# Optimization experiments

Measured on AMD Instinct MI355X. Metric: run time of the kernel, lower is better.

Reference implementation:

```python
import jax, jax.numpy as jnp
import numpy as np

N = 100000
E = 1600000
IN_F, HID, OUT = 64, 128, 64


def setup_inputs() -> dict:
    key = jax.random.key(0)
    ks = jax.random.split(key, 16)
    glorot = lambda k, shp: jax.random.normal(k, shp, jnp.float32) * (2.0 / (shp[0] + shp[1])) ** 0.5
    return {
        "features": jax.random.normal(ks[0], (N, IN_F), jnp.float32),
        "W_neigh1": glorot(ks[1], (IN_F, HID)),
        "W_self1": glorot(ks[2], (IN_F, HID)),
        "b1": jnp.zeros((HID,), jnp.float32),
        "W_neigh2": glorot(ks[3], (HID, HID)),
        "W_self2": glorot(ks[4], (HID, HID)),
        "b2": jnp.zeros((HID,), jnp.float32),
        "Wm1": glorot(ks[5], (HID, HID)),
        "bm1": jnp.zeros((HID,), jnp.float32),
        "Wm2": glorot(ks[6], (HID, OUT)),
        "bm2": jnp.zeros((OUT,), jnp.float32),
        "src": jax.random.randint(ks[7], (E,), 0, N, jnp.int64),
        "dst": jax.random.randint(ks[8], (E,), 0, N, jnp.int64),
    }


def _sage_conv(x, src, dst, W_neigh, W_self, b):
    # mean aggregation of in-neighbor messages (DGL SAGEConv 'mean')
    msg = x[src]                                            # [E, d]
    agg = jax.ops.segment_sum(msg, dst, num_segments=N)     # [N, d]
    deg = jax.ops.segment_sum(jnp.ones((E,), x.dtype), dst, num_segments=N)
    h_neigh = agg / jnp.maximum(deg, 1.0)[:, None]
    return x @ W_self + h_neigh @ W_neigh + b


def reference(features, W_neigh1, W_self1, b1, W_neigh2, W_self2, b2,
              Wm1, bm1, Wm2, bm2, src, dst):
    x = jax.nn.relu(_sage_conv(features, src, dst, W_neigh1, W_self1, b1))
    x = jax.nn.relu(_sage_conv(x, src, dst, W_neigh2, W_self2, b2))
    x = jax.nn.relu(x @ Wm1 + bm1)
    return x @ Wm2 + bm2
```

## Files before the change

kernel.cpp:

```cpp
#include <hip/hip_runtime.h>
#include <hip/hip_fp8.h>

#define N_IN 64
#define HID 128
#define OUT_F 64
#define EPB 6144
#define BKT 128

typedef unsigned short ushort_t;
typedef unsigned char  uchar_t;
typedef unsigned long long ull_t;
typedef ushort_t us8  __attribute__((ext_vector_type(8)));
typedef uchar_t  uc8  __attribute__((ext_vector_type(8)));
typedef short    s16x8 __attribute__((ext_vector_type(8)));
typedef float    f32x4 __attribute__((ext_vector_type(4)));
typedef unsigned int uint2v __attribute__((ext_vector_type(2)));

__device__ inline ushort_t f2bf(float f) {
    unsigned u = __float_as_uint(f);
    u = u + 0x7fffu + ((u >> 16) & 1u);
    return (ushort_t)(u >> 16);
}
__device__ inline float bf2f(ushort_t b) {
    return __uint_as_float((unsigned)b << 16);
}
__device__ inline uchar_t f2fp8(float v) {
    __hip_fp8_e4m3 q(v);
    return (uchar_t)q.__x;
}
__device__ inline void fp8x4_to_f32(unsigned int dw, float* o) {
#if __has_builtin(__builtin_amdgcn_cvt_pk_f32_fp8)
    auto lo = __builtin_amdgcn_cvt_pk_f32_fp8(dw, false);
    auto hi = __builtin_amdgcn_cvt_pk_f32_fp8(dw, true);
    o[0] = lo[0]; o[1] = lo[1]; o[2] = hi[0]; o[3] = hi[1];
#else
#pragma unroll
    for (int i = 0; i < 4; ++i) {
        __hip_fp8_e4m3 h; h.__x = (dw >> (8 * i)) & 0xff;
        o[i] = (float)h;
    }
#endif
}

__global__ __launch_bounds__(256)
void prep_kernel(const float* __restrict__ feat, ushort_t* __restrict__ featb,
                 uchar_t* __restrict__ featq, int n8,
                 const float* __restrict__ Ws1, const float* __restrict__ Wn1,
                 const float* __restrict__ Ws2, const float* __restrict__ Wn2,
                 const float* __restrict__ Wm1, const float* __restrict__ Wm2,
                 ushort_t* __restrict__ wsT1, ushort_t* __restrict__ wnT1,
                 ushort_t* __restrict__ wsT2, ushort_t* __restrict__ wnT2,
                 ushort_t* __restrict__ wmT1, ushort_t* __restrict__ wmT2,
                 const int* __restrict__ dst, int* __restrict__ histT,
                 int E, int nbuk, int nba, int BA, int BB) {
    __shared__ int hist[800];
    int b = blockIdx.x;
    int tid = threadIdx.x;
    if (b < BA) {
        int i = b * 256 + tid;
        if (i >= n8) return;
        f32x4 a = ((const f32x4*)feat)[2 * i];
        f32x4 c = ((const f32x4*)feat)[2 * i + 1];
        us8 v; uc8 q;
#pragma unroll
        for (int t = 0; t < 4; ++t) {
            v[t] = f2bf(a[t]); v[4 + t] = f2bf(c[t]);
            q[t] = f2fp8(a[t]); q[4 + t] = f2fp8(c[t]);
        }
        ((us8*)featb)[i] = v;
        ((uc8*)featq)[i] = q;
    } else if (b < BB) {
        int i = (b - BA) * 256 + tid;
        const float* W; ushort_t* WT; int K, H, l;
        if      (i < 8192)  { W = Ws1; WT = wsT1; K = 64;  H = 128; l = i; }
        else if (i < 16384) { W = Wn1; WT = wnT1; K = 64;  H = 128; l = i - 8192; }
        else if (i < 32768) { W = Ws2; WT = wsT2; K = 128; H = 128; l = i - 16384; }
        else if (i < 49152) { W = Wn2; WT = wnT2; K = 128; H = 128; l = i - 32768; }
        else if (i < 65536) { W = Wm1; WT = wmT1; K = 128; H = 128; l = i - 49152; }
        else if (i < 73728) { W = Wm2; WT = wmT2; K = 128; H = 64;  l = i - 65536; }
        else return;
        int h = l / K, k = l % K;
        WT[l] = f2bf(W[(size_t)k * H + h]);
    } else {
        const int blk  = b - BB;
        const int base = blk * EPB;
        for (int k = tid; k < nbuk; k += 256) hist[k] = 0;
        __syncthreads();
#pragma unroll
        for (int it = 0; it < EPB / 256; ++it) {
            int e = base + it * 256 + tid;
            if (e < E) atomicAdd(&hist[(unsigned)dst[e] / BKT], 1);
        }
        __syncthreads();
        for (int k = tid; k < nbuk; k += 256)
            histT[(size_t)k * nba + blk] = hist[k];
    }
}

__global__ __launch_bounds__(256)
void scan_block(const int* __restrict__ in, int* __restrict__ out,
                int* __restrict__ partials, int n) {
    __shared__ int sm[256];
    int i = blockIdx.x * 256 + threadIdx.x;
    int v = (i < n) ? in[i] : 0;
    sm[threadIdx.x] = v;
    __syncthreads();
    for (int d = 1; d < 256; d <<= 1) {
        int t = (threadIdx.x >= d) ? sm[threadIdx.x - d] : 0;
        __syncthreads();
        sm[threadIdx.x] += t;
        __syncthreads();
    }
    if (i < n) out[i] = sm[threadIdx.x] - v;
    if (threadIdx.x == 255) partials[blockIdx.x] = sm[255];
}

__global__ __launch_bounds__(1024)
void scan_partials(int* __restrict__ partials, int nparts) {
    __shared__ int sm[1024];
    int i = threadIdx.x;
    int v = (i < nparts) ? partials[i] : 0;
    sm[i] = v;
    __syncthreads();
    for (int d = 1; d < 1024; d <<= 1) {
        int t = (i >= d) ? sm[i - d] : 0;
        __syncthreads();
        sm[i] += t;
        __syncthreads();
    }
    if (i < nparts) partials[i] = sm[i] - v;
}

__global__ __launch_bounds__(256)
void scan_add(int* __restrict__ arr, const int* __restrict__ partials, int n) {
    int i = blockIdx.x * 256 + threadIdx.x;
    if (i < n) arr[i] += partials[i >> 8];
}

__global__ __launch_bounds__(256)
void part_edges(const int* __restrict__ src, const int* __restrict__ dst,
                const int* __restrict__ histT, ull_t* __restrict__ ebsd,
                int E, int nbuk, int nba) {
    __shared__ int cur[800];
    const int blk  = blockIdx.x;
    const int base = blk * EPB;
    const int tid  = threadIdx.x;
    for (int k = tid; k < nbuk; k += 256)
        cur[k] = histT[(size_t)k * nba + blk];
    __syncthreads();
#pragma unroll
    for (int it = 0; it < EPB / 256; ++it) {
        int e = base + it * 256 + tid;
        if (e < E) {
            int d = dst[e], s = src[e];
            int pos = atomicAdd(&cur[(unsigned)d / BKT], 1);
            ebsd[pos] = (ull_t)(unsigned)s | ((ull_t)(unsigned)d << 32);
        }
    }
}

__global__ __launch_bounds__(256)
void build_bucket(const ull_t* __restrict__ ebsd, const int* __restrict__ histT,
                  int* __restrict__ offs, float* __restrict__ invd,
                  int* __restrict__ csr_src, int nn, int E, int nbuk, int nba) {
    __shared__ int sm[BKT];
    __shared__ int cur[BKT];
    const int b   = blockIdx.x;
    const int b0  = b * BKT;
    const int tid = threadIdx.x;
    const int ebase = histT[(size_t)b * nba];
    const int eend  = (b == nbuk - 1) ? E : histT[(size_t)(b + 1) * nba];

    if (tid < BKT) sm[tid] = 0;
    __syncthreads();
    for (int j = ebase + tid; j < eend; j += 256) {
        int d = (int)(ebsd[j] >> 32);
        atomicAdd(&sm[d - b0], 1);
    }
    __syncthreads();
    const int deg = (tid < BKT) ? sm[tid] : 0;
    for (int d = 1; d < BKT; d <<= 1) {
        int t = (tid >= d && tid < BKT) ? sm[tid - d] : 0;
        __syncthreads();
        if (tid < BKT) sm[tid] += t;
        __syncthreads();
    }
    if (tid < BKT) {
        const int excl = sm[tid] - deg;
        const int n = b0 + tid;
        if (n < nn) {
            offs[n] = ebase + excl;
            invd[n] = 1.0f / fmaxf((float)deg, 1.0f);
        }
        if (b == nbuk - 1 && tid == 0) offs[nn] = E;
        cur[tid] = ebase + excl;
    }
    __syncthreads();
    for (int j = ebase + tid; j < eend; j += 256) {
        ull_t p = ebsd[j];
        int s = (int)(unsigned)p;
        int d = (int)(p >> 32);
        int pos = atomicAdd(&cur[d - b0], 1);
        csr_src[pos] = s;
    }
}

template<int D>
__global__ __launch_bounds__(256)
void gather_fp8(const uchar_t* __restrict__ xq, const int* __restrict__ csr_src,
                const int* __restrict__ offs, const float* __restrict__ invd,
                ushort_t* __restrict__ aggb, int nn) {
    constexpr int C  = D / 8;
    constexpr int NE = 64 / C;
    const int n = (blockIdx.x * 256 + threadIdx.x) >> 6;
    if (n >= nn) return;
    const int lane = threadIdx.x & 63;
    const int c  = lane % C;
    const int eg = lane / C;
    const uchar_t* tab = xq + (size_t)c * 8;

    const int beg = offs[n], end = offs[n + 1];
    float acc[8] = {0.f, 0.f, 0.f, 0.f, 0.f, 0.f, 0.f, 0.f};

    int j = beg + eg;
    for (; j + NE < end; j += 2 * NE) {
        int s0 = csr_src[j], s1 = csr_src[j + NE];
        uint2v q0 = *(const uint2v*)(tab + (size_t)s0 * D);
        uint2v q1 = *(const uint2v*)(tab + (size_t)s1 * D);
        float f0[8], f1[8];
        fp8x4_to_f32(q0[0], f0); fp8x4_to_f32(q0[1], f0 + 4);
        fp8x4_to_f32(q1[0], f1); fp8x4_to_f32(q1[1], f1 + 4);
#pragma unroll
        for (int t = 0; t < 8; ++t) acc[t] += f0[t] + f1[t];
    }
    if (j < end) {
        int s = csr_src[j];
        uint2v q = *(const uint2v*)(tab + (size_t)s * D);
        float f[8];
        fp8x4_to_f32(q[0], f); fp8x4_to_f32(q[1], f + 4);
#pragma unroll
        for (int t = 0; t < 8; ++t) acc[t] += f[t];
    }

#pragma unroll
    for (int m = C; m < 64; m <<= 1) {
#pragma unroll
        for (int t = 0; t < 8; ++t) acc[t] += __shfl_xor(acc[t], m, 64);
    }

    if (eg == 0) {
        float iv = invd[n];
        us8 ov;
#pragma unroll
        for (int t = 0; t < 8; ++t) ov[t] = f2bf(acc[t] * iv);
        *(us8*)(aggb + (size_t)n * D + c * 8) = ov;
    }
}

template<int K, int H, bool NEIGH, bool RELU, bool OBF, bool OFP8>
__global__ __launch_bounds__(256)
void mfma_layer(const ushort_t* __restrict__ xb, const ushort_t* __restrict__ gb,
                const ushort_t* __restrict__ wsT, const ushort_t* __restrict__ wnT,
                const float* __restrict__ bias, void* __restrict__ out,
                uchar_t* __restrict__ outq, int nn) {
    constexpr int CH   = K / 8;
    constexpr int KS   = K / 32;
    constexpr int WTPW = H / 64;
    constexpr int PF   = CH / 4;

    __shared__ us8 xs[64][CH];
    __shared__ us8 gs[NEIGH ? 64 : 1][NEIGH ? CH : 1];

    const int tid  = threadIdx.x;
    const int lane = tid & 63;
    const int w    = tid >> 6;
    const int lr   = lane & 15;
    const int lk   = lane >> 4;

    s16x8 bws[WTPW][KS];
    s16x8 bwn[NEIGH ? WTPW : 1][NEIGH ? KS : 1];
#pragma unroll
    for (int t = 0; t < WTPW; ++t) {
        const size_t hrow = (size_t)((w * WTPW + t) * 16 + lr) * K;
#pragma unroll
        for (int ks = 0; ks < KS; ++ks) {
            bws[t][ks] = *(const s16x8*)(wsT + hrow + ks * 32 + lk * 8);
            if constexpr (NEIGH)
                bwn[t][ks] = *(const s16x8*)(wnT + hrow + ks * 32 + lk * 8);
        }
    }
    float bv[WTPW];
#pragma unroll
    for (int t = 0; t < WTPW; ++t) bv[t] = bias[(w * WTPW + t) * 16 + lr];

    const int ntiles = (nn + 63) >> 6;
    us8 pfx[PF], pfg[NEIGH ? PF : 1];
    const us8 z8 = {0, 0, 0, 0, 0, 0, 0, 0};

    auto loadpf = [&](int T) {
        const int base = T * 64;
#pragma unroll
        for (int q = 0; q < PF; ++q) {
            int idx = tid + q * 256, r = idx / CH, c = idx % CH, n = base + r;
            pfx[q] = (n < nn) ? *(const us8*)(xb + (size_t)n * K + c * 8) : z8;
            if constexpr (NEIGH)
                pfg[q] = (n < nn) ? *(const us8*)(gb + (size_t)n * K + c * 8) : z8;
        }
    };

    int tile = blockIdx.x;
    if (tile >= ntiles) return;
    loadpf(tile);

    while (true) {
        __syncthreads();
#pragma unroll
        for (int q = 0; q < PF; ++q) {
            int idx = tid + q * 256, r = idx / CH, c = idx % CH;
            int cs = c ^ (r & 7);
            xs[r][cs] = pfx[q];
            if constexpr (NEIGH) gs[r][cs] = pfg[q];
        }
        __syncthreads();

        const int row0 = tile * 64;
        tile += gridDim.x;
        if (tile < ntiles) loadpf(tile);

        f32x4 acc[4][WTPW];
#pragma unroll
        for (int rg = 0; rg < 4; ++rg)
#pragma unroll
            for (int t = 0; t < WTPW; ++t) acc[rg][t] = {0.f, 0.f, 0.f, 0.f};

#pragma unroll
        for (int rg = 0; rg < 4; ++rg) {
            const int R = rg * 16 + lr;
#pragma unroll
            for (int ks = 0; ks < KS; ++ks) {
                const int cs = (ks * 4 + lk) ^ (R & 7);
                s16x8 ax = (s16x8)xs[R][cs];
                s16x8 ag;
                if constexpr (NEIGH) ag = (s16x8)gs[R][cs];
#pragma unroll
                for (int t = 0; t < WTPW; ++t) {
                    acc[rg][t] = __builtin_amdgcn_mfma_f32_16x16x32_bf16(ax, bws[t][ks], acc[rg][t], 0, 0, 0);
                    if constexpr (NEIGH)
                        acc[rg][t] = __builtin_amdgcn_mfma_f32_16x16x32_bf16(ag, bwn[t][ks], acc[rg][t], 0, 0, 0);
                }
            }
        }

#pragma unroll
        for (int rg = 0; rg < 4; ++rg) {
#pragma unroll
            for (int t = 0; t < WTPW; ++t) {
                const int h = (w * WTPW + t) * 16 + lr;
#pragma unroll
                for (int j = 0; j < 4; ++j) {
                    int n = row0 + rg * 16 + lk * 4 + j;
                    if (n < nn) {
                        float v = acc[rg][t][j] + bv[t];
                        if constexpr (RELU) v = fmaxf(v, 0.f);
                        if constexpr (OBF)
                            ((ushort_t*)out)[(size_t)n * H + h] = f2bf(v);
                        else
                            ((float*)out)[(size_t)n * H + h] = v;
                        if constexpr (OFP8)
                            outq[(size_t)n * H + h] = f2fp8(v);
                    }
                }
            }
        }

        if (tile >= ntiles) break;
    }
}

extern "C" void kernel_launch(void* const* d_in, const int* in_sizes, int n_in,
                              void* d_out, int out_size, void* d_ws, size_t ws_size,
                              hipStream_t stream) {
    const float* feat = (const float*)d_in[0];
    const float* Wn1  = (const float*)d_in[1];
    const float* Ws1  = (const float*)d_in[2];
    const float* b1   = (const float*)d_in[3];
    const float* Wn2  = (const float*)d_in[4];
    const float* Ws2  = (const float*)d_in[5];
    const float* b2   = (const float*)d_in[6];
    const float* Wm1  = (const float*)d_in[7];
    const float* bm1  = (const float*)d_in[8];
    const float* Wm2  = (const float*)d_in[9];
    const float* bm2  = (const float*)d_in[10];
    const int*   src  = (const int*)d_in[11];
    const int*   dst  = (const int*)d_in[12];

    const int nn = in_sizes[0] / N_IN;
    const int E  = in_sizes[11];

    const int nbuk  = (nn + BKT - 1) / BKT;
    const int nba   = (E + EPB - 1) / EPB;
    const int nhist = nbuk * nba;

    char* p = (char*)d_ws;
    auto alloc = [&](size_t bytes) { void* q = p; p += (bytes + 63) & ~(size_t)63; return q; };
    int*      offs     = (int*)alloc((size_t)(nn + 1) * 4);
    int*      partials = (int*)alloc(1024 * 4);
    float*    invd     = (float*)alloc((size_t)nn * 4);
    int*      histT    = (int*)alloc((size_t)nhist * 4);
    ull_t*    ebsd     = (ull_t*)alloc((size_t)E * 8);
    int*      csr_src  = (int*)alloc((size_t)E * 4);
    ushort_t* wsT1     = (ushort_t*)alloc((size_t)N_IN * HID * 2);
    ushort_t* wnT1     = (ushort_t*)alloc((size_t)N_IN * HID * 2);
    ushort_t* wsT2     = (ushort_t*)alloc((size_t)HID * HID * 2);
    ushort_t* wnT2     = (ushort_t*)alloc((size_t)HID * HID * 2);
    ushort_t* wmT1     = (ushort_t*)alloc((size_t)HID * HID * 2);
    ushort_t* wmT2     = (ushort_t*)alloc((size_t)HID * OUT_F * 2);
    ushort_t* featb    = (ushort_t*)alloc((size_t)nn * N_IN * 2);
    uchar_t*  x1q      = (uchar_t*)alloc((size_t)nn * HID);
    ushort_t* x2b      = featb;
    ushort_t* x1b      = (ushort_t*)alloc((size_t)nn * HID * 2);
    ushort_t* x3b      = x1b;
    ushort_t* agg2b    = (ushort_t*)alloc((size_t)nn * HID * 2);
    ushort_t* agg1b    = (ushort_t*)d_out;
    uchar_t*  featq    = (uchar_t*)d_out + (size_t)nn * N_IN * 2;

    const int ntiles = (nn + 63) / 64;
    const int NB     = ntiles < 768 ? ntiles : 768;
    const int n8     = nn * (N_IN / 8);
    const int BA     = (n8 + 255) / 256;
    const int BB     = BA + (73728 + 255) / 256;
    const int BC     = BB + nba;

    prep_kernel<<<BC, 256, 0, stream>>>(
        feat, featb, featq, n8,
        Ws1, Wn1, Ws2, Wn2, Wm1, Wm2,
        wsT1, wnT1, wsT2, wnT2, wmT1, wmT2,
        dst, histT, E, nbuk, nba, BA, BB);

    const int nparts = (nhist + 255) / 256;
    scan_block<<<nparts, 256, 0, stream>>>(histT, histT, partials, nhist);
    scan_partials<<<1, 1024, 0, stream>>>(partials, nparts);
    scan_add<<<nparts, 256, 0, stream>>>(histT, partials, nhist);

    part_edges<<<nba, 256, 0, stream>>>(src, dst, histT, ebsd, E, nbuk, nba);
    build_bucket<<<nbuk, 256, 0, stream>>>(ebsd, histT, offs, invd, csr_src, nn, E, nbuk, nba);

    gather_fp8<N_IN><<<(nn + 3) / 4, 256, 0, stream>>>(
        featq, csr_src, offs, invd, agg1b, nn);
    mfma_layer<N_IN, HID, true, true, true, true><<<NB, 256, 0, stream>>>(
        featb, agg1b, wsT1, wnT1, b1, x1b, x1q, nn);

    gather_fp8<HID><<<(nn + 3) / 4, 256, 0, stream>>>(
        x1q, csr_src, offs, invd, agg2b, nn);
    mfma_layer<HID, HID, true, true, true, false><<<NB, 256, 0, stream>>>(
        x1b, agg2b, wsT2, wnT2, b2, x2b, nullptr, nn);

    mfma_layer<HID, HID, false, true, true, false><<<NB, 256, 0, stream>>>(
        x2b, nullptr, wmT1, nullptr, bm1, x3b, nullptr, nn);
    mfma_layer<HID, OUT_F, false, false, false, false><<<NB, 256, 0, stream>>>(
        x3b, nullptr, wmT2, nullptr, bm2, (float*)d_out, nullptr, nn);
}
```

Measured before the change: 208.9 us.

## Fuse layer-2 SAGE and MLP head into one MFMA kernel; unroll gather by four

The second SAGE layer, the hidden MLP layer and the output layer now run in a single persistent kernel. Each 64-row tile stays in LDS as bf16 between the three matmuls, so the two intermediate activation tensors are never written to or read back from global memory, and two launches go away. The fused kernel holds all four weight sets in registers, which raises register pressure and may lower occupancy; the grid is capped at 512 blocks. The fp8 gather loop is also unrolled to four edges per iteration with packed float2 accumulation, giving more loads in flight.

After: 208.3 us. No clear change (-0.3%).

```diff
diff --git a/kernel.cpp b/kernel.cpp
--- a/kernel.cpp
+++ b/kernel.cpp
@@ -14,6 +14,7 @@
 typedef uchar_t  uc8  __attribute__((ext_vector_type(8)));
 typedef short    s16x8 __attribute__((ext_vector_type(8)));
 typedef float    f32x4 __attribute__((ext_vector_type(4)));
+typedef float    f32x2 __attribute__((ext_vector_type(2)));
 typedef unsigned int uint2v __attribute__((ext_vector_type(2)));
 
 __device__ inline ushort_t f2bf(float f) {
@@ -28,17 +29,20 @@
     __hip_fp8_e4m3 q(v);
     return (uchar_t)q.__x;
 }
-__device__ inline void fp8x4_to_f32(unsigned int dw, float* o) {
+template<bool HI>
+__device__ inline f32x2 fp8pair(unsigned int dw) {
 #if __has_builtin(__builtin_amdgcn_cvt_pk_f32_fp8)
-    auto lo = __builtin_amdgcn_cvt_pk_f32_fp8(dw, false);
-    auto hi = __builtin_amdgcn_cvt_pk_f32_fp8(dw, true);
-    o[0] = lo[0]; o[1] = lo[1]; o[2] = hi[0]; o[3] = hi[1];
+    auto r = __builtin_amdgcn_cvt_pk_f32_fp8(dw, HI);
+    f32x2 o; o[0] = r[0]; o[1] = r[1];
+    return o;
 #else
-#pragma unroll
-    for (int i = 0; i < 4; ++i) {
-        __hip_fp8_e4m3 h; h.__x = (dw >> (8 * i)) & 0xff;
+    f32x2 o;
+#pragma unroll
+    for (int i = 0; i < 2; ++i) {
+        __hip_fp8_e4m3 h; h.__x = (dw >> (8 * (2 * (int)HI + i))) & 0xff;
         o[i] = (float)h;
     }
+    return o;
 #endif
 }
 
@@ -220,39 +224,55 @@
     const uchar_t* tab = xq + (size_t)c * 8;
 
     const int beg = offs[n], end = offs[n + 1];
-    float acc[8] = {0.f, 0.f, 0.f, 0.f, 0.f, 0.f, 0.f, 0.f};
+    f32x2 acc[4];
+#pragma unroll
+    for (int t = 0; t < 4; ++t) acc[t] = (f32x2){0.f, 0.f};
 
     int j = beg + eg;
-    for (; j + NE < end; j += 2 * NE) {
-        int s0 = csr_src[j], s1 = csr_src[j + NE];
+    for (; j + 3 * NE < end; j += 4 * NE) {
+        int s0 = csr_src[j],          s1 = csr_src[j + NE];
+        int s2 = csr_src[j + 2 * NE], s3 = csr_src[j + 3 * NE];
         uint2v q0 = *(const uint2v*)(tab + (size_t)s0 * D);
         uint2v q1 = *(const uint2v*)(tab + (size_t)s1 * D);
-        float f0[8], f1[8];
-        fp8x4_to_f32(q0[0], f0); fp8x4_to_f32(q0[1], f0 + 4);
-        fp8x4_to_f32(q1[0], f1); fp8x4_to_f32(q1[1], f1 + 4);
-#pragma unroll
-        for (int t = 0; t < 8; ++t) acc[t] += f0[t] + f1[t];
-    }
-    if (j < end) {
+        uint2v q2 = *(const uint2v*)(tab + (size_t)s2 * D);
+        uint2v q3 = *(const uint2v*)(tab + (size_t)s3 * D);
+#pragma unroll
+        for (int d = 0; d < 2; ++d) {
+            f32x2 l01 = fp8pair<false>(q0[d]) + fp8pair<false>(q1[d]);
+            f32x2 l23 = fp8pair<false>(q2[d]) + fp8pair<false>(q3[d]);
+            acc[2 * d] += l01 + l23;
+            f32x2 h01 = fp8pair<true>(q0[d]) + fp8pair<true>(q1[d]);
+            f32x2 h23 = fp8pair<true>(q2[d]) + fp8pair<true>(q3[d]);
+            acc[2 * d + 1] += h01 + h23;
+        }
+    }
+    for (; j < end; j += NE) {
         int s = csr_src[j];
         uint2v q = *(const uint2v*)(tab + (size_t)s * D);
-        float f[8];
-        fp8x4_to_f32(q[0], f); fp8x4_to_f32(q[1], f + 4);
-#pragma unroll
-        for (int t = 0; t < 8; ++t) acc[t] += f[t];
+#pragma unroll
+        for (int d = 0; d < 2; ++d) {
+            acc[2 * d]     += fp8pair<false>(q[d]);
+            acc[2 * d + 1] += fp8pair<true>(q[d]);
+        }
     }
 
 #pragma unroll
     for (int m = C; m < 64; m <<= 1) {
 #pragma unroll
-        for (int t = 0; t < 8; ++t) acc[t] += __shfl_xor(acc[t], m, 64);
+        for (int t = 0; t < 4; ++t) {
+            acc[t][0] += __shfl_xor(acc[t][0], m, 64);
+            acc[t][1] += __shfl_xor(acc[t][1], m, 64);
+        }
     }
 
     if (eg == 0) {
         float iv = invd[n];
         us8 ov;
 #pragma unroll
-        for (int t = 0; t < 8; ++t) ov[t] = f2bf(acc[t] * iv);
+        for (int t = 0; t < 4; ++t) {
+            ov[2 * t]     = f2bf(acc[t][0] * iv);
+            ov[2 * t + 1] = f2bf(acc[t][1] * iv);
+        }
         *(us8*)(aggb + (size_t)n * D + c * 8) = ov;
     }
 }
@@ -372,6 +392,175 @@
                 }
             }
         }
+
+        if (tile >= ntiles) break;
+    }
+}
+
+__global__ __launch_bounds__(256)
+void mfma_tail(const ushort_t* __restrict__ xb, const ushort_t* __restrict__ gb,
+               const ushort_t* __restrict__ wsT2, const ushort_t* __restrict__ wnT2,
+               const ushort_t* __restrict__ wmT1, const ushort_t* __restrict__ wmT2,
+               const float* __restrict__ b2, const float* __restrict__ bm1,
+               const float* __restrict__ bm2, float* __restrict__ out, int nn) {
+    constexpr int CH = 16, KS = 4, PF = 4;
+    __shared__ us8 xs[64][CH];
+    __shared__ us8 gs[64][CH];
+    ushort_t* xs16 = (ushort_t*)xs;
+    ushort_t* gs16 = (ushort_t*)gs;
+
+    const int tid  = threadIdx.x;
+    const int lane = tid & 63;
+    const int w    = tid >> 6;
+    const int lr   = lane & 15;
+    const int lk   = lane >> 4;
+
+    s16x8 bws2[2][KS], bwn2[2][KS], bwm1[2][KS], bwm2[KS];
+#pragma unroll
+    for (int t = 0; t < 2; ++t) {
+        const size_t hrow = (size_t)((w * 2 + t) * 16 + lr) * HID;
+#pragma unroll
+        for (int ks = 0; ks < KS; ++ks) {
+            bws2[t][ks] = *(const s16x8*)(wsT2 + hrow + ks * 32 + lk * 8);
+            bwn2[t][ks] = *(const s16x8*)(wnT2 + hrow + ks * 32 + lk * 8);
+            bwm1[t][ks] = *(const s16x8*)(wmT1 + hrow + ks * 32 + lk * 8);
+        }
+    }
+    {
+        const size_t hrow = (size_t)(w * 16 + lr) * HID;
+#pragma unroll
+        for (int ks = 0; ks < KS; ++ks)
+            bwm2[ks] = *(const s16x8*)(wmT2 + hrow + ks * 32 + lk * 8);
+    }
+    float bv2[2]  = {b2[(w * 2) * 16 + lr],  b2[(w * 2 + 1) * 16 + lr]};
+    float bvm1[2] = {bm1[(w * 2) * 16 + lr], bm1[(w * 2 + 1) * 16 + lr]};
+    float bvm2    = bm2[w * 16 + lr];
+
+    const int ntiles = (nn + 63) >> 6;
+    us8 pfx[PF], pfg[PF];
+    const us8 z8 = {0, 0, 0, 0, 0, 0, 0, 0};
+
+    auto loadpf = [&](int T) {
+        const int base = T * 64;
+#pragma unroll
+        for (int q = 0; q < PF; ++q) {
+            int idx = tid + q * 256, r = idx / CH, c = idx % CH, n = base + r;
+            pfx[q] = (n < nn) ? *(const us8*)(xb + (size_t)n * HID + c * 8) : z8;
+            pfg[q] = (n < nn) ? *(const us8*)(gb + (size_t)n * HID + c * 8) : z8;
+        }
+    };
+
+    auto st_bf = [&](ushort_t* base, int r, int h, float v) {
+        int c8 = h >> 3, e = h & 7;
+        int cs = c8 ^ (r & 7);
+        base[r * 128 + cs * 8 + e] = f2bf(v);
+    };
+
+    int tile = blockIdx.x;
+    if (tile >= ntiles) return;
+    loadpf(tile);
+
+    while (true) {
+        __syncthreads();
+#pragma unroll
+        for (int q = 0; q < PF; ++q) {
+            int idx = tid + q * 256, r = idx / CH, c = idx % CH;
+            int cs = c ^ (r & 7);
+            xs[r][cs] = pfx[q];
+            gs[r][cs] = pfg[q];
+        }
+        __syncthreads();
+
+        const int row0 = tile * 64;
+        tile += gridDim.x;
+        if (tile < ntiles) loadpf(tile);
+
+        f32x4 a1[4][2];
+#pragma unroll
+        for (int rg = 0; rg < 4; ++rg)
+#pragma unroll
+            for (int t = 0; t < 2; ++t) a1[rg][t] = {0.f, 0.f, 0.f, 0.f};
+#pragma unroll
+        for (int rg = 0; rg < 4; ++rg) {
+            const int R = rg * 16 + lr;
+#pragma unroll
+            for (int ks = 0; ks < KS; ++ks) {
+                const int cs = (ks * 4 + lk) ^ (R & 7);
+                s16x8 ax = (s16x8)xs[R][cs];
+                s16x8 ag = (s16x8)gs[R][cs];
+#pragma unroll
+                for (int t = 0; t < 2; ++t) {
+                    a1[rg][t] = __builtin_amdgcn_mfma_f32_16x16x32_bf16(ax, bws2[t][ks], a1[rg][t], 0, 0, 0);
+                    a1[rg][t] = __builtin_amdgcn_mfma_f32_16x16x32_bf16(ag, bwn2[t][ks], a1[rg][t], 0, 0, 0);
+                }
+            }
+        }
+        __syncthreads();
+#pragma unroll
+        for (int rg = 0; rg < 4; ++rg)
+#pragma unroll
+            for (int t = 0; t < 2; ++t) {
+                const int h = (w * 2 + t) * 16 + lr;
+#pragma unroll
+                for (int j = 0; j < 4; ++j) {
+                    int r = rg * 16 + lk * 4 + j;
+                    st_bf(gs16, r, h, fmaxf(a1[rg][t][j] + bv2[t], 0.f));
+                }
+            }
+        __syncthreads();
+
+        f32x4 a2[4][2];
+#pragma unroll
+        for (int rg = 0; rg < 4; ++rg)
+#pragma unroll
+            for (int t = 0; t < 2; ++t) a2[rg][t] = {0.f, 0.f, 0.f, 0.f};
+#pragma unroll
+        for (int rg = 0; rg < 4; ++rg) {
+            const int R = rg * 16 + lr;
+#pragma unroll
+            for (int ks = 0; ks < KS; ++ks) {
+                const int cs = (ks * 4 + lk) ^ (R & 7);
+                s16x8 ax = (s16x8)gs[R][cs];
+#pragma unroll
+                for (int t = 0; t < 2; ++t)
+                    a2[rg][t] = __builtin_amdgcn_mfma_f32_16x16x32_bf16(ax, bwm1[t][ks], a2[rg][t], 0, 0, 0);
+            }
+        }
+        __syncthreads();
+#pragma unroll
+        for (int rg = 0; rg < 4; ++rg)
+#pragma unroll
+            for (int t = 0; t < 2; ++t) {
+                const int h = (w * 2 + t) * 16 + lr;
+#pragma unroll
+                for (int j = 0; j < 4; ++j) {
+                    int r = rg * 16 + lk * 4 + j;
+                    st_bf(xs16, r, h, fmaxf(a2[rg][t][j] + bvm1[t], 0.f));
+                }
+            }
+        __syncthreads();
+
+        f32x4 a3[4];
+#pragma unroll
+        for (int rg = 0; rg < 4; ++rg) a3[rg] = {0.f, 0.f, 0.f, 0.f};
+#pragma unroll
+        for (int rg = 0; rg < 4; ++rg) {
+            const int R = rg * 16 + lr;
+#pragma unroll
+            for (int ks = 0; ks < KS; ++ks) {
+                const int cs = (ks * 4 + lk) ^ (R & 7);
+                s16x8 ax = (s16x8)xs[R][cs];
+                a3[rg] = __builtin_amdgcn_mfma_f32_16x16x32_bf16(ax, bwm2[ks], a3[rg], 0, 0, 0);
+            }
+        }
+        const int h3 = w * 16 + lr;
+#pragma unroll
+        for (int rg = 0; rg < 4; ++rg)
+#pragma unroll
+            for (int j = 0; j < 4; ++j) {
+                int n = row0 + rg * 16 + lk * 4 + j;
+                if (n < nn) out[(size_t)n * OUT_F + h3] = a3[rg][j] + bvm2;
+            }
 
         if (tile >= ntiles) break;
     }
@@ -417,15 +606,14 @@
     ushort_t* wmT2     = (ushort_t*)alloc((size_t)HID * OUT_F * 2);
     ushort_t* featb    = (ushort_t*)alloc((size_t)nn * N_IN * 2);
     uchar_t*  x1q      = (uchar_t*)alloc((size_t)nn * HID);
-    ushort_t* x2b      = featb;
     ushort_t* x1b      = (ushort_t*)alloc((size_t)nn * HID * 2);
-    ushort_t* x3b      = x1b;
     ushort_t* agg2b    = (ushort_t*)alloc((size_t)nn * HID * 2);
     ushort_t* agg1b    = (ushort_t*)d_out;
     uchar_t*  featq    = (uchar_t*)d_out + (size_t)nn * N_IN * 2;
 
     const int ntiles = (nn + 63) / 64;
     const int NB     = ntiles < 768 ? ntiles : 768;
+    const int NBT    = ntiles < 512 ? ntiles : 512;
     const int n8     = nn * (N_IN / 8);
     const int BA     = (n8 + 255) / 256;
     const int BB     = BA + (73728 + 255) / 256;
@@ -452,11 +640,7 @@
 
     gather_fp8<HID><<<(nn + 3) / 4, 256, 0, stream>>>(
         x1q, csr_src, offs, invd, agg2b, nn);
-    mfma_layer<HID, HID, true, true, true, false><<<NB, 256, 0, stream>>>(
-        x1b, agg2b, wsT2, wnT2, b2, x2b, nullptr, nn);
-
-    mfma_layer<HID, HID, false, true, true, false><<<NB, 256, 0, stream>>>(
-        x2b, nullptr, wmT1, nullptr, bm1, x3b, nullptr, nn);
-    mfma_layer<HID, OUT_F, false, false, false, false><<<NB, 256, 0, stream>>>(
-        x3b, nullptr, wmT2, nullptr, bm2, (float*)d_out, nullptr, nn);
-}
+
+    mfma_tail<<<NBT, 256, 0, stream>>>(
+        x1b, agg2b, wsT2, wnT2, wmT1, wmT2, b2, bm1, bm2, (float*)d_out, nn);
+}
```
